# Kernel optimization log

Measured on AMD Instinct MI355X. Metric: run time of the kernel, lower is better.

## Reference

```python
import jax, jax.numpy as jnp
import numpy as np
from jax import lax

RADIUS = 4
SIGMA_1 = 5.0
SIGMA_2 = 1.0


def _gaussian_kernel_3d(radius, sigma):
    x = np.linspace(-radius, radius, 2 * radius + 1)
    xx, yy, zz = np.meshgrid(x, x, x)
    dist2 = xx ** 2 + yy ** 2 + zz ** 2
    k = np.exp(-dist2 / (2.0 * sigma ** 2)).astype(np.float32)
    return jnp.asarray(k)[None, None]  # [O=1, I=1, D, H, W]


def _conv3d_same(x, kernel, radius):
    # x: [B,1,D,H,W], kernel: [1,1,kd,kh,kw]
    pad = [(radius, radius)] * 3
    return lax.conv_general_dilated(
        x, kernel, window_strides=(1, 1, 1), padding=pad,
        dimension_numbers=('NCDHW', 'OIDHW', 'NCDHW'))


def setup_inputs() -> dict:
    key = jax.random.key(0)
    k1, k2 = jax.random.split(key)
    labels = jax.random.uniform(k1, (4, 1, 160, 160, 160), dtype=jnp.float32)
    inputs = jax.random.uniform(k2, (4, 1, 160, 160, 160), dtype=jnp.float32)
    return {"labels": labels, "inputs": inputs}


def reference(labels, inputs):
    kernel = _gaussian_kernel_3d(RADIUS, SIGMA_1)
    num_classes = 2
    p0 = labels[:, 0:1]  # [B,1,D,H,W]
    loss = jnp.float32(0.0)
    for k in range(num_classes):
        class_probs = p0 if k == 0 else 1.0 - p0
        class_mean = (jnp.mean(inputs * class_probs, axis=(2, 3, 4), keepdims=True)
                      / (jnp.mean(class_probs, axis=(2, 3, 4), keepdims=True) + 1e-5))
        diff = jnp.sum((inputs - class_mean) ** 2, axis=1, keepdims=True)  # [B,1,D,H,W]
        weights = jnp.exp(-(diff ** 2) / (SIGMA_2 ** 2))
        numerator = jnp.sum(class_probs * _conv3d_same(class_probs * weights, kernel, RADIUS))
        denominator = jnp.sum(class_probs * _conv3d_same(weights, kernel, RADIUS))
        # L1Loss(scalar, 0) == abs(scalar)
        loss = loss + jnp.abs(numerator / (denominator + 1e-6))
    return jnp.float32(num_classes) - loss
```

## Files before the change

### kernel.cpp

```cpp
#include <hip/hip_runtime.h>
#include <math.h>

#define NX   160
#define N2   25600
#define N3   4096000
#define NB   4

#define NBLK_S 2048
#define SBLK_PER_B 512
#define F4_PER_BLK 2000

#define XT   8
#define XTP  10
#define YT   32
#define ZCH  20
#define SROWS 40
#define NBLK_F 800

__device__ __constant__ float G1[9] = {
    0.72614903f, 0.83527021f, 0.92311635f, 0.98019867f, 1.0f,
    0.98019867f, 0.92311635f, 0.83527021f, 0.72614903f};

#define ES_FULL 7.92946852f
__device__ __constant__ float ES_M[4] = {3.46473426f, 2.48453559f, 1.56141924f,
                                         0.72614903f};
__device__ inline float edge_sum(int i) {
    float s = ES_FULL;
    if (i < 4) s -= ES_M[i];
    if (i > NX - 5) s -= ES_M[NX - 1 - i];
    return s;
}

__device__ inline float4 f4_zero() { return make_float4(0.f, 0.f, 0.f, 0.f); }
__device__ inline float4 f4_axpy(float a, float4 b, float4 c) {
    return make_float4(c.x + a * b.x, c.y + a * b.y, c.z + a * b.z, c.w + a * b.w);
}

template <int NV>
__device__ inline void block_reduce_store(double* vals, double* dst) {
    __shared__ double red[4][NV];
    int lane = threadIdx.x & 63;
    int wave = threadIdx.x >> 6;
#pragma unroll
    for (int v = 0; v < NV; ++v) {
        double x = vals[v];
#pragma unroll
        for (int off = 32; off > 0; off >>= 1) x += __shfl_down(x, off, 64);
        if (lane == 0) red[wave][v] = x;
    }
    __syncthreads();
    if (threadIdx.x < NV) {
        int v = threadIdx.x;
        dst[v] = red[0][v] + red[1][v] + red[2][v] + red[3][v];
    }
}

__global__ __launch_bounds__(256) void sums_kernel(
    const float* __restrict__ labels, const float* __restrict__ inputs,
    double* __restrict__ pS) {
    int blk = blockIdx.x;
    int b = blk >> 9;
    int chunk = blk & 511;
    const float4* lp = (const float4*)(labels + b * N3) + chunk * F4_PER_BLK;
    const float4* ip = (const float4*)(inputs + b * N3) + chunk * F4_PER_BLK;
    double sp = 0.0, sip = 0.0, si = 0.0;
    for (int i = threadIdx.x; i < F4_PER_BLK; i += 256) {
        float4 p = lp[i];
        float4 in = ip[i];
        sp += (double)(p.x + p.y + p.z + p.w);
        sip += (double)(in.x * p.x + in.y * p.y + in.z * p.z + in.w * p.w);
        si += (double)(in.x + in.y + in.z + in.w);
    }
    double vals[3] = {sp, sip, si};
    block_reduce_store<3>(vals, pS + 3 * blk);
}

__device__ inline void load_row_raw(const float* __restrict__ lbase, int zp,
                                    int gy, int gc, float4* r) {
    bool ok = (zp >= 0) && (zp < NX) && (gy >= 0) && (gy < NX);
    const float* row = lbase + zp * N2 + gy * NX;
#pragma unroll
    for (int c = 0; c < 3; ++c) {
        int g4 = gc - 1 + c;
        r[c] = (ok && g4 >= 0 && g4 < 40) ? *(const float4*)&row[4 * g4]
                                          : f4_zero();
    }
}

__device__ inline float4 xconv_regs(const float4* r) {
    float w[12] = {r[0].x, r[0].y, r[0].z, r[0].w, r[1].x, r[1].y,
                   r[1].z, r[1].w, r[2].x, r[2].y, r[2].z, r[2].w};
    float4 o = f4_zero();
#pragma unroll
    for (int kk = 0; kk < 9; ++kk) {
        float g = G1[kk];
        o.x += g * w[kk];     o.y += g * w[kk + 1];
        o.z += g * w[kk + 2]; o.w += g * w[kk + 3];
    }
    return o;
}

__device__ inline float4 ydot9(const float4 (*sb)[XTP], int oy, int ox) {
    float4 w8 = f4_zero();
#pragma unroll
    for (int dy = 0; dy < 9; ++dy) w8 = f4_axpy(G1[dy], sb[oy + dy][ox], w8);
    return w8;
}

__global__ __launch_bounds__(256, 4) void fused_conv_kernel(
    const float* __restrict__ labels, const float* __restrict__ inputs,
    const double* __restrict__ pS, double* __restrict__ pZ) {
    int tid = threadIdx.x;
    int xcd = blockIdx.x & 7;
    int u = blockIdx.x >> 3;
    int xt = u % 5;
    int yt = (u / 5) % 5;
    int b = u / 25;
    int x0f = xt * XT;
    int y0 = yt * YT;
    int z0 = xcd * 20;

    __shared__ float sM[2];
    {
        double v0 = 0, v1 = 0, v2 = 0;
        for (int i = tid; i < SBLK_PER_B; i += 256) {
            const double* p = pS + 3 * (SBLK_PER_B * b + i);
            v0 += p[0]; v1 += p[1]; v2 += p[2];
        }
        __shared__ double red[4][3];
        int lane = tid & 63, wave = tid >> 6;
        double vals[3] = {v0, v1, v2};
#pragma unroll
        for (int v = 0; v < 3; ++v) {
            double x = vals[v];
#pragma unroll
            for (int off = 32; off > 0; off >>= 1) x += __shfl_down(x, off, 64);
            if (lane == 0) red[wave][v] = x;
        }
        __syncthreads();
        if (tid == 0) {
            double sp = red[0][0] + red[1][0] + red[2][0] + red[3][0];
            double sip = red[0][1] + red[1][1] + red[2][1] + red[3][1];
            double si = red[0][2] + red[1][2] + red[2][2] + red[3][2];
            const double Nv = (double)N3;
            sM[0] = (float)((sip / Nv) / (sp / Nv + 1e-5));
            sM[1] = (float)(((si - sip) / Nv) / ((Nv - sp) / Nv + 1e-5));
        }
        __syncthreads();
    }
    float m0 = sM[0], m1 = sM[1];

    int ox = tid & 7;
    int oy = tid >> 3;
    int y = y0 + oy;
    int xo = (x0f + ox) * 4;
    float ey = edge_sum(y);
    float cx[4] = {edge_sum(xo) * ey, edge_sum(xo + 1) * ey,
                   edge_sum(xo + 2) * ey, edge_sum(xo + 3) * ey};

    const float* lbase = labels + b * N3;
    const float* ibase = inputs + b * N3;
    int po = y * NX + xo;

    int sra = tid >> 3, sca = tid & 7;
    int srb = 32 + (tid >> 3), scb = tid & 7;
    bool hasb = (tid < 64);
    int gya = y0 - 4 + sra, gyb = y0 - 4 + srb;
    int gca = x0f + sca, gcb = x0f + scb;

    __shared__ float4 sbuf[2][SROWS][XTP];

    {
        float4 ra[3], rb[3];
        load_row_raw(lbase, z0 - 4, gya, gca, ra);
        if (hasb) load_row_raw(lbase, z0 - 4, gyb, gcb, rb);
        sbuf[0][sra][sca] = xconv_regs(ra);
        if (hasb) sbuf[0][srb][scb] = xconv_regs(rb);
    }
    __syncthreads();

    float4 win[9];
#pragma unroll
    for (int d = 0; d < 9; ++d) win[d] = f4_zero();

    float n0 = 0.f, d0 = 0.f, n1 = 0.f, d1 = 0.f;
    for (int k = 0; k < ZCH + 8; ++k) {
        int cur = k & 1, nxt = cur ^ 1;
        int zstage = z0 - 4 + k + 1;

        float4 ra[3], rb[3];
        load_row_raw(lbase, zstage, gya, gca, ra);
        if (hasb) load_row_raw(lbase, zstage, gyb, gcb, rb);

        int z = z0 + k - 8;
        float4 pv = f4_zero(), iv = f4_zero();
        if (k >= 8) {
            pv = *(const float4*)&lbase[z * N2 + po];
            iv = *(const float4*)&ibase[z * N2 + po];
        }

        float4 w8 = ydot9(sbuf[cur], oy, ox);

#pragma unroll
        for (int d = 0; d < 8; ++d) win[d] = win[d + 1];
        win[8] = w8;

        if (k >= 8) {
            float4 c4 = f4_zero();
#pragma unroll
            for (int d = 0; d < 9; ++d) c4 = f4_axpy(G1[d], win[d], c4);
            float ez = edge_sum(z);
            float pc[4] = {pv.x, pv.y, pv.z, pv.w};
            float ic[4] = {iv.x, iv.y, iv.z, iv.w};
            float cc[4] = {c4.x, c4.y, c4.z, c4.w};
#pragma unroll
            for (int l = 0; l < 4; ++l) {
                float c1 = cx[l] * ez - cc[l];
                float df0 = ic[l] - m0; df0 *= df0;
                float w0 = __expf(-df0 * df0);
                float df1 = ic[l] - m1; df1 *= df1;
                float w1 = __expf(-df1 * df1);
                n0 += cc[l] * pc[l] * w0;
                d0 += cc[l] * w0;
                n1 += c1 * (1.f - pc[l]) * w1;
                d1 += c1 * w1;
            }
        }

        float4 oa = xconv_regs(ra);
        sbuf[nxt][sra][sca] = oa;
        if (hasb) {
            float4 ob = xconv_regs(rb);
            sbuf[nxt][srb][scb] = ob;
        }

        __syncthreads();
    }
    double vals[4] = {(double)n0, (double)d0, (double)n1, (double)d1};
    block_reduce_store<4>(vals, pZ + 4 * blockIdx.x);
}

__global__ __launch_bounds__(256) void finalize_kernel(
    const double* __restrict__ pZ, float* __restrict__ out) {
    double a0 = 0, a1 = 0, a2 = 0, a3 = 0;
    for (int i = threadIdx.x; i < NBLK_F; i += 256) {
        const double* p = &pZ[4 * i];
        a0 += p[0]; a1 += p[1]; a2 += p[2]; a3 += p[3];
    }
    __shared__ double red[4][4];
    int lane = threadIdx.x & 63;
    int wave = threadIdx.x >> 6;
    double vals[4] = {a0, a1, a2, a3};
#pragma unroll
    for (int v = 0; v < 4; ++v) {
        double x = vals[v];
#pragma unroll
        for (int off = 32; off > 0; off >>= 1) x += __shfl_down(x, off, 64);
        if (lane == 0) red[wave][v] = x;
    }
    __syncthreads();
    if (threadIdx.x == 0) {
        double acc[4];
#pragma unroll
        for (int v = 0; v < 4; ++v)
            acc[v] = red[0][v] + red[1][v] + red[2][v] + red[3][v];
        double r0 = fabs(acc[0] / (acc[1] + 1e-6));
        double r1 = fabs(acc[2] / (acc[3] + 1e-6));
        out[0] = (float)(2.0 - r0 - r1);
    }
}

extern "C" void kernel_launch(void* const* d_in, const int* in_sizes, int n_in,
                              void* d_out, int out_size, void* d_ws, size_t ws_size,
                              hipStream_t stream) {
    const float* labels = (const float*)d_in[0];
    const float* inputs = (const float*)d_in[1];
    float* out = (float*)d_out;

    double* pS = (double*)d_ws;
    double* pZ = (double*)((char*)d_ws + 192128);

    hipLaunchKernelGGL(sums_kernel, dim3(NBLK_S), dim3(256), 0, stream,
                       labels, inputs, pS);
    hipLaunchKernelGGL(fused_conv_kernel, dim3(NBLK_F), dim3(256), 0, stream,
                       labels, inputs, pS, pZ);
    hipLaunchKernelGGL(finalize_kernel, dim3(1), dim3(256), 0, stream, pZ, out);
}
```

Measured before the change: 243.5 us.

## Merge three kernels into one persistent kernel with grid barrier and atomics

Folds the statistics pass, the fused convolution and the finalize step into one kernel of 1600 blocks. Per-batch sums are accumulated with double atomics and the blocks wait at a spin-wait grid barrier, and the last block to finish computes the output through a counter. The z chunk is halved so there are twice as many conv blocks, and the occupancy hint is raised to 7. This removes two kernel launches and the partial-sum buffers, but a spin barrier relies on all 1600 blocks being resident at once, and atomics on a few addresses add contention.

Measured after the change: 670.2 us. +175.2%, slower.

```diff
diff --git a/kernel.cpp b/kernel.cpp
--- a/kernel.cpp
+++ b/kernel.cpp
@@ -6,16 +6,15 @@
 #define N3   4096000
 #define NB   4
 
-#define NBLK_S 2048
-#define SBLK_PER_B 512
-#define F4_PER_BLK 2000
+#define NBLK 1600
+#define ABLK_PER_B 400
+#define AF4  2560
 
 #define XT   8
 #define XTP  10
 #define YT   32
-#define ZCH  20
+#define ZCH  10
 #define SROWS 40
-#define NBLK_F 800
 
 __device__ __constant__ float G1[9] = {
     0.72614903f, 0.83527021f, 0.92311635f, 0.98019867f, 1.0f,
@@ -37,7 +36,7 @@
 }
 
 template <int NV>
-__device__ inline void block_reduce_store(double* vals, double* dst) {
+__device__ inline void block_reduce_atomic(double* vals, double* dst) {
     __shared__ double red[4][NV];
     int lane = threadIdx.x & 63;
     int wave = threadIdx.x >> 6;
@@ -50,29 +49,12 @@
     }
     __syncthreads();
     if (threadIdx.x < NV) {
-        int v = threadIdx.x;
-        dst[v] = red[0][v] + red[1][v] + red[2][v] + red[3][v];
-    }
-}
-
-__global__ __launch_bounds__(256) void sums_kernel(
-    const float* __restrict__ labels, const float* __restrict__ inputs,
-    double* __restrict__ pS) {
-    int blk = blockIdx.x;
-    int b = blk >> 9;
-    int chunk = blk & 511;
-    const float4* lp = (const float4*)(labels + b * N3) + chunk * F4_PER_BLK;
-    const float4* ip = (const float4*)(inputs + b * N3) + chunk * F4_PER_BLK;
-    double sp = 0.0, sip = 0.0, si = 0.0;
-    for (int i = threadIdx.x; i < F4_PER_BLK; i += 256) {
-        float4 p = lp[i];
-        float4 in = ip[i];
-        sp += (double)(p.x + p.y + p.z + p.w);
-        sip += (double)(in.x * p.x + in.y * p.y + in.z * p.z + in.w * p.w);
-        si += (double)(in.x + in.y + in.z + in.w);
-    }
-    double vals[3] = {sp, sip, si};
-    block_reduce_store<3>(vals, pS + 3 * blk);
+        double part = red[0][threadIdx.x] + red[1][threadIdx.x] +
+                      red[2][threadIdx.x] + red[3][threadIdx.x];
+        double old = atomicAdd(&dst[threadIdx.x], part);
+        asm volatile("" :: "v"(old));
+    }
+    __syncthreads();
 }
 
 __device__ inline void load_row_raw(const float* __restrict__ lbase, int zp,
@@ -107,48 +89,63 @@
     return w8;
 }
 
-__global__ __launch_bounds__(256, 4) void fused_conv_kernel(
+__global__ __launch_bounds__(256, 7) void mono_kernel(
     const float* __restrict__ labels, const float* __restrict__ inputs,
-    const double* __restrict__ pS, double* __restrict__ pZ) {
+    double* __restrict__ SA, double* __restrict__ Z,
+    unsigned int* __restrict__ cntA, unsigned int* __restrict__ cntB,
+    float* __restrict__ out) {
     int tid = threadIdx.x;
-    int xcd = blockIdx.x & 7;
-    int u = blockIdx.x >> 3;
+    int bid = blockIdx.x;
+
+    {
+        int ab = bid / ABLK_PER_B;
+        int chunk = bid % ABLK_PER_B;
+        const float4* lp = (const float4*)(labels + ab * N3) + chunk * AF4;
+        const float4* ip = (const float4*)(inputs + ab * N3) + chunk * AF4;
+        double sp = 0.0, sip = 0.0, si = 0.0;
+        for (int i = tid; i < AF4; i += 256) {
+            float4 p = lp[i];
+            float4 in = ip[i];
+            sp += (double)(p.x + p.y + p.z + p.w);
+            sip += (double)(in.x * p.x + in.y * p.y + in.z * p.z + in.w * p.w);
+            si += (double)(in.x + in.y + in.z + in.w);
+        }
+        double vals[3] = {sp, sip, si};
+        block_reduce_atomic<3>(vals, SA + 3 * ab);
+        if (tid == 0) {
+            unsigned int o = atomicAdd(cntA, 1u);
+            asm volatile("" :: "v"(o));
+            while (__hip_atomic_load(cntA, __ATOMIC_RELAXED,
+                                     __HIP_MEMORY_SCOPE_AGENT) < NBLK)
+                __builtin_amdgcn_s_sleep(8);
+        }
+        __syncthreads();
+    }
+
+    __shared__ float sM[2];
+    int u = bid >> 3;
+    int xcd = bid & 7;
     int xt = u % 5;
     int yt = (u / 5) % 5;
-    int b = u / 25;
+    int zs = (u / 25) % 2;
+    int b = u / 50;
+    if (tid == 0) {
+        double sp = __hip_atomic_load(&SA[3 * b + 0], __ATOMIC_RELAXED,
+                                      __HIP_MEMORY_SCOPE_AGENT);
+        double sip = __hip_atomic_load(&SA[3 * b + 1], __ATOMIC_RELAXED,
+                                       __HIP_MEMORY_SCOPE_AGENT);
+        double si = __hip_atomic_load(&SA[3 * b + 2], __ATOMIC_RELAXED,
+                                      __HIP_MEMORY_SCOPE_AGENT);
+        const double Nv = (double)N3;
+        sM[0] = (float)((sip / Nv) / (sp / Nv + 1e-5));
+        sM[1] = (float)(((si - sip) / Nv) / ((Nv - sp) / Nv + 1e-5));
+    }
+    __syncthreads();
+    float m0 = sM[0], m1 = sM[1];
+
     int x0f = xt * XT;
     int y0 = yt * YT;
-    int z0 = xcd * 20;
-
-    __shared__ float sM[2];
-    {
-        double v0 = 0, v1 = 0, v2 = 0;
-        for (int i = tid; i < SBLK_PER_B; i += 256) {
-            const double* p = pS + 3 * (SBLK_PER_B * b + i);
-            v0 += p[0]; v1 += p[1]; v2 += p[2];
-        }
-        __shared__ double red[4][3];
-        int lane = tid & 63, wave = tid >> 6;
-        double vals[3] = {v0, v1, v2};
-#pragma unroll
-        for (int v = 0; v < 3; ++v) {
-            double x = vals[v];
-#pragma unroll
-            for (int off = 32; off > 0; off >>= 1) x += __shfl_down(x, off, 64);
-            if (lane == 0) red[wave][v] = x;
-        }
-        __syncthreads();
-        if (tid == 0) {
-            double sp = red[0][0] + red[1][0] + red[2][0] + red[3][0];
-            double sip = red[0][1] + red[1][1] + red[2][1] + red[3][1];
-            double si = red[0][2] + red[1][2] + red[2][2] + red[3][2];
-            const double Nv = (double)N3;
-            sM[0] = (float)((sip / Nv) / (sp / Nv + 1e-5));
-            sM[1] = (float)(((si - sip) / Nv) / ((Nv - sp) / Nv + 1e-5));
-        }
-        __syncthreads();
-    }
-    float m0 = sM[0], m1 = sM[1];
+    int z0 = xcd * 20 + zs * ZCH;
 
     int ox = tid & 7;
     int oy = tid >> 3;
@@ -233,40 +230,26 @@
             float4 ob = xconv_regs(rb);
             sbuf[nxt][srb][scb] = ob;
         }
-
         __syncthreads();
     }
+
     double vals[4] = {(double)n0, (double)d0, (double)n1, (double)d1};
-    block_reduce_store<4>(vals, pZ + 4 * blockIdx.x);
-}
-
-__global__ __launch_bounds__(256) void finalize_kernel(
-    const double* __restrict__ pZ, float* __restrict__ out) {
-    double a0 = 0, a1 = 0, a2 = 0, a3 = 0;
-    for (int i = threadIdx.x; i < NBLK_F; i += 256) {
-        const double* p = &pZ[4 * i];
-        a0 += p[0]; a1 += p[1]; a2 += p[2]; a3 += p[3];
-    }
-    __shared__ double red[4][4];
-    int lane = threadIdx.x & 63;
-    int wave = threadIdx.x >> 6;
-    double vals[4] = {a0, a1, a2, a3};
-#pragma unroll
-    for (int v = 0; v < 4; ++v) {
-        double x = vals[v];
-#pragma unroll
-        for (int off = 32; off > 0; off >>= 1) x += __shfl_down(x, off, 64);
-        if (lane == 0) red[wave][v] = x;
-    }
-    __syncthreads();
-    if (threadIdx.x == 0) {
-        double acc[4];
-#pragma unroll
-        for (int v = 0; v < 4; ++v)
-            acc[v] = red[0][v] + red[1][v] + red[2][v] + red[3][v];
-        double r0 = fabs(acc[0] / (acc[1] + 1e-6));
-        double r1 = fabs(acc[2] / (acc[3] + 1e-6));
-        out[0] = (float)(2.0 - r0 - r1);
+    block_reduce_atomic<4>(vals, Z);
+    if (tid == 0) {
+        unsigned int o = atomicAdd(cntB, 1u);
+        if (o == NBLK - 1) {
+            double a0 = __hip_atomic_load(&Z[0], __ATOMIC_RELAXED,
+                                          __HIP_MEMORY_SCOPE_AGENT);
+            double a1 = __hip_atomic_load(&Z[1], __ATOMIC_RELAXED,
+                                          __HIP_MEMORY_SCOPE_AGENT);
+            double a2 = __hip_atomic_load(&Z[2], __ATOMIC_RELAXED,
+                                          __HIP_MEMORY_SCOPE_AGENT);
+            double a3 = __hip_atomic_load(&Z[3], __ATOMIC_RELAXED,
+                                          __HIP_MEMORY_SCOPE_AGENT);
+            double r0 = fabs(a0 / (a1 + 1e-6));
+            double r1 = fabs(a2 / (a3 + 1e-6));
+            out[0] = (float)(2.0 - r0 - r1);
+        }
     }
 }
 
@@ -277,12 +260,13 @@
     const float* inputs = (const float*)d_in[1];
     float* out = (float*)d_out;
 
-    double* pS = (double*)d_ws;
-    double* pZ = (double*)((char*)d_ws + 192128);
-
-    hipLaunchKernelGGL(sums_kernel, dim3(NBLK_S), dim3(256), 0, stream,
-                       labels, inputs, pS);
-    hipLaunchKernelGGL(fused_conv_kernel, dim3(NBLK_F), dim3(256), 0, stream,
-                       labels, inputs, pS, pZ);
-    hipLaunchKernelGGL(finalize_kernel, dim3(1), dim3(256), 0, stream, pZ, out);
-}
+    double* SA = (double*)d_ws;
+    double* Z = (double*)((char*)d_ws + 96);
+    unsigned int* cntA = (unsigned int*)((char*)d_ws + 128);
+    unsigned int* cntB = (unsigned int*)((char*)d_ws + 132);
+
+    hipMemsetAsync(d_ws, 0, 192, stream);
+
+    hipLaunchKernelGGL(mono_kernel, dim3(NBLK), dim3(256), 0, stream,
+                       labels, inputs, SA, Z, cntA, cntB, out);
+}
```
